# Optimization experiments

Measured on AMD Instinct MI355X. Metric: run time of the kernel, lower is better.

Reference implementation:

```python
import jax, jax.numpy as jnp
import numpy as np

B, C, H, W = 16, 512, 64, 64
K = 32


def setup_inputs() -> dict:
    key = jax.random.key(0)
    k1, k2, k3 = jax.random.split(key, 3)
    std = 1.0 / (64 * C) ** 0.5
    x = jax.random.normal(k1, (B, C, H, W), dtype=jnp.float32)
    codewords = jax.random.uniform(k2, (K, C), dtype=jnp.float32, minval=-std, maxval=std)
    scale = jax.random.uniform(k3, (K,), dtype=jnp.float32, minval=-1.0, maxval=0.0)
    return {"x": x, "codewords": codewords, "scale": scale}


def reference(x, codewords, scale):
    b, c, h, w = x.shape
    # (b, n, c) with n = h*w spatial positions
    xf = x.reshape(b, c, h * w).transpose(0, 2, 1)
    x2 = jnp.sum(xf * xf, axis=-1)                       # (b, n)
    c2 = jnp.sum(codewords * codewords, axis=-1)          # (k,)
    xc = jnp.einsum('bnc,kc->bnk', xf, codewords)         # (b, n, k)
    logits = scale[None, None, :] * (x2[:, :, None] - 2.0 * xc + c2[None, None, :])
    A = jax.nn.softmax(logits, axis=2)                    # (b, n, k)
    # sum_n A[b,n,k] * (x[b,n,c] - codewords[k,c])
    encoded = jnp.einsum('bnk,bnc->bkc', A, xf) - jnp.einsum('bnk,kc->bkc', A, codewords)
    return encoded
```

## Files before the change

kernel.cpp:

```cpp
#include <hip/hip_runtime.h>
#include <hip/hip_bf16.h>
#include <math.h>

#define BB 16
#define CC 512
#define NN 4096
#define KK 32

typedef __attribute__((ext_vector_type(8))) short short8;
typedef __attribute__((ext_vector_type(4))) float float4v;

static __device__ __forceinline__ unsigned short f2bf(float f) {
  unsigned u = __float_as_uint(f);
  u += 0x7FFF + ((u >> 16) & 1);
  return (unsigned short)(u >> 16);
}


__global__ __launch_bounds__(256) void prep_kernel(
    const float* __restrict__ cw, unsigned short* __restrict__ cwB,
    float* __restrict__ c2, float* __restrict__ asum, float* __restrict__ out) {
  int gid = blockIdx.x * 256 + threadIdx.x;
  float4v z = {0.f, 0.f, 0.f, 0.f};
  float4v* o4 = (float4v*)out;
#pragma unroll
  for (int j = 0; j < 4; ++j) o4[gid + j * 16384] = z;
  if (gid < BB * KK) asum[gid] = 0.f;
  cwB[gid] = f2bf(cw[gid]);
  __shared__ float c2p[KK][8];
  if (blockIdx.x == 0) {
    int k = threadIdx.x >> 3, j = threadIdx.x & 7;
    const float* row = cw + k * CC + j * 64;
    float s = 0.f;
    for (int i = 0; i < 64; ++i) s = fmaf(row[i], row[i], s);
    c2p[k][j] = s;
    __syncthreads();
    if (threadIdx.x < KK) {
      float t = 0.f;
      for (int j2 = 0; j2 < 8; ++j2) t += c2p[threadIdx.x][j2];
      c2[threadIdx.x] = t;
    }
  }
}

__global__ __launch_bounds__(256, 2) void logits_kernel(
    const float* __restrict__ x, const unsigned short* __restrict__ cwB,
    const float* __restrict__ c2g, const float* __restrict__ scale,
    unsigned short* __restrict__ A, float* __restrict__ asum) {
  const int b = blockIdx.x >> 6;
  const int n0 = (blockIdx.x & 63) << 6;
  const int t = threadIdx.x;

  __shared__ unsigned short Xl[512][68];
  __shared__ float Sx2p[16][68];
  __shared__ float Sx2[64];

  const float* xb = x + (size_t)b * CC * NN + n0;

  {
    const int f4 = t & 15;
    const int cr = t >> 4;
    float x2p0 = 0.f, x2p1 = 0.f, x2p2 = 0.f, x2p3 = 0.f;
    for (int cc = 0; cc < 512; cc += 64) {
      float4v v[4];
#pragma unroll
      for (int i = 0; i < 4; ++i)
        v[i] = *(const float4v*)(xb + (size_t)(cc + 16 * i + cr) * NN + 4 * f4);
#pragma unroll
      for (int i = 0; i < 4; ++i) {
        x2p0 = fmaf(v[i].x, v[i].x, x2p0);
        x2p1 = fmaf(v[i].y, v[i].y, x2p1);
        x2p2 = fmaf(v[i].z, v[i].z, x2p2);
        x2p3 = fmaf(v[i].w, v[i].w, x2p3);
        unsigned short h0 = f2bf(v[i].x), h1 = f2bf(v[i].y);
        unsigned short h2 = f2bf(v[i].z), h3 = f2bf(v[i].w);
        unsigned p0 = (unsigned)h0 | ((unsigned)h1 << 16);
        unsigned p1 = (unsigned)h2 | ((unsigned)h3 << 16);
        uint2 pk = make_uint2(p0, p1);
        *(uint2*)&Xl[cc + 16 * i + cr][4 * f4] = pk;
      }
    }
    Sx2p[cr][4 * f4 + 0] = x2p0;
    Sx2p[cr][4 * f4 + 1] = x2p1;
    Sx2p[cr][4 * f4 + 2] = x2p2;
    Sx2p[cr][4 * f4 + 3] = x2p3;
  }
  __syncthreads();
  if (t < 64) {
    float s = 0.f;
#pragma unroll
    for (int r = 0; r < 16; ++r) s += Sx2p[r][t];
    Sx2[t] = s;
  }
  __syncthreads();

  const int w = t >> 6;
  const int l = t & 63;
  const int l15 = l & 15;
  const int q = l >> 4;
  const int nrow = w * 16 + l15;

  float4v acc0 = {0.f, 0.f, 0.f, 0.f};
  float4v acc1 = {0.f, 0.f, 0.f, 0.f};

  for (int cs = 0; cs < 512; cs += 32) {
    const int cb = cs + q * 8;
    short8 af;
#pragma unroll
    for (int j = 0; j < 8; ++j) af[j] = (short)Xl[cb + j][nrow];
    short8 b0 = *(const short8*)(cwB + (size_t)l15 * CC + cb);
    short8 b1 = *(const short8*)(cwB + (size_t)(16 + l15) * CC + cb);
    acc0 = __builtin_amdgcn_mfma_f32_16x16x32_bf16(af, b0, acc0, 0, 0, 0);
    acc1 = __builtin_amdgcn_mfma_f32_16x16x32_bf16(af, b1, acc1, 0, 0, 0);
  }

  const float sc0 = scale[l15], sc1 = scale[16 + l15];
  const float cc0 = c2g[l15], cc1 = c2g[16 + l15];

  float a0[4], a1[4];
#pragma unroll
  for (int r = 0; r < 4; ++r) {
    const float xx = Sx2[w * 16 + 4 * q + r];
    float l0 = sc0 * (xx - 2.f * acc0[r] + cc0);
    float l1 = sc1 * (xx - 2.f * acc1[r] + cc1);
    float m = fmaxf(l0, l1);
    m = fmaxf(m, __shfl_xor(m, 1));
    m = fmaxf(m, __shfl_xor(m, 2));
    m = fmaxf(m, __shfl_xor(m, 4));
    m = fmaxf(m, __shfl_xor(m, 8));
    float e0 = __expf(l0 - m), e1 = __expf(l1 - m);
    float s = e0 + e1;
    s += __shfl_xor(s, 1);
    s += __shfl_xor(s, 2);
    s += __shfl_xor(s, 4);
    s += __shfl_xor(s, 8);
    float inv = 1.0f / s;
    a0[r] = e0 * inv;
    a1[r] = e1 * inv;
  }

  {
    unsigned p00 = (unsigned)f2bf(a0[0]) | ((unsigned)f2bf(a0[1]) << 16);
    unsigned p01 = (unsigned)f2bf(a0[2]) | ((unsigned)f2bf(a0[3]) << 16);
    unsigned p10 = (unsigned)f2bf(a1[0]) | ((unsigned)f2bf(a1[1]) << 16);
    unsigned p11 = (unsigned)f2bf(a1[2]) | ((unsigned)f2bf(a1[3]) << 16);
    unsigned short* A0 = A + ((size_t)(b * KK + l15)) * NN + n0 + w * 16 + 4 * q;
    unsigned short* A1 = A + ((size_t)(b * KK + 16 + l15)) * NN + n0 + w * 16 + 4 * q;
    *(uint2*)A0 = make_uint2(p00, p01);
    *(uint2*)A1 = make_uint2(p10, p11);
  }

  {
    float s0 = a0[0] + a0[1] + a0[2] + a0[3];
    float s1 = a1[0] + a1[1] + a1[2] + a1[3];
    s0 += __shfl_xor(s0, 16);
    s0 += __shfl_xor(s0, 32);
    s1 += __shfl_xor(s1, 16);
    s1 += __shfl_xor(s1, 32);
    if (q == 0) {
      atomicAdd(&asum[b * KK + l15], s0);
      atomicAdd(&asum[b * KK + 16 + l15], s1);
    }
  }
}

__global__ __launch_bounds__(256, 4) void agg_kernel(
    const float* __restrict__ x, const unsigned short* __restrict__ A,
    float* __restrict__ out) {
  const int b = blockIdx.x >> 6;
  const int cg = (blockIdx.x >> 4) & 3;
  const int n0 = (blockIdx.x & 15) << 8;
  const int t = threadIdx.x;
  const int w = t >> 6;
  const int l = t & 63;
  const int l15 = l & 15;
  const int q = l >> 4;
  const int cw0 = cg * 128 + 32 * w;

  float4v acc[2][2];
#pragma unroll
  for (int ct = 0; ct < 2; ++ct)
#pragma unroll
    for (int m = 0; m < 2; ++m) acc[ct][m] = (float4v){0.f, 0.f, 0.f, 0.f};

  const unsigned short* Ab = A + (size_t)b * KK * NN;
  const float* xb = x + (size_t)b * CC * NN;

  for (int s = 0; s < 8; ++s) {
    const int nb = n0 + s * 32 + q * 8;
    short8 a0 = *(const short8*)(Ab + (size_t)l15 * NN + nb);
    short8 a1 = *(const short8*)(Ab + (size_t)(16 + l15) * NN + nb);
#pragma unroll
    for (int ct = 0; ct < 2; ++ct) {
      const int c = cw0 + 16 * ct + l15;
      const float* xp = xb + (size_t)c * NN + nb;
      float4v x0 = *(const float4v*)xp;
      float4v x1 = *(const float4v*)(xp + 4);
      short8 bv;
      bv[0] = (short)f2bf(x0.x);
      bv[1] = (short)f2bf(x0.y);
      bv[2] = (short)f2bf(x0.z);
      bv[3] = (short)f2bf(x0.w);
      bv[4] = (short)f2bf(x1.x);
      bv[5] = (short)f2bf(x1.y);
      bv[6] = (short)f2bf(x1.z);
      bv[7] = (short)f2bf(x1.w);
      acc[ct][0] = __builtin_amdgcn_mfma_f32_16x16x32_bf16(a0, bv, acc[ct][0], 0, 0, 0);
      acc[ct][1] = __builtin_amdgcn_mfma_f32_16x16x32_bf16(a1, bv, acc[ct][1], 0, 0, 0);
    }
  }

#pragma unroll
  for (int ct = 0; ct < 2; ++ct) {
    const int c = cw0 + 16 * ct + l15;
#pragma unroll
    for (int m = 0; m < 2; ++m)
#pragma unroll
      for (int r = 0; r < 4; ++r) {
        int k = 16 * m + 4 * q + r;
        atomicAdd(&out[((size_t)(b * KK + k)) * CC + c], acc[ct][m][r]);
      }
  }
}

__global__ __launch_bounds__(256) void finalize_kernel(
    float* __restrict__ out, const float* __restrict__ asum,
    const float* __restrict__ cw) {
  int idx = blockIdx.x * 256 + threadIdx.x;
  int b = idx >> 12;
  int k = (idx >> 7) & 31;
  int c4 = idx & 127;
  float4v o = ((float4v*)out)[idx];
  float4v wv = ((const float4v*)cw)[k * 128 + c4];
  float a = asum[b * KK + k];
  o.x -= a * wv.x;
  o.y -= a * wv.y;
  o.z -= a * wv.z;
  o.w -= a * wv.w;
  ((float4v*)out)[idx] = o;
}

extern "C" void kernel_launch(void* const* d_in, const int* in_sizes, int n_in,
                              void* d_out, int out_size, void* d_ws, size_t ws_size,
                              hipStream_t stream) {
  const float* x = (const float*)d_in[0];
  const float* cw = (const float*)d_in[1];
  const float* scale = (const float*)d_in[2];
  float* out = (float*)d_out;
  char* ws = (char*)d_ws;

  float* c2 = (float*)ws;
  unsigned short* cwB = (unsigned short*)(ws + 128);
  float* asum = (float*)(ws + 32896);
  unsigned short* A = (unsigned short*)(ws + 34944);

  prep_kernel<<<64, 256, 0, stream>>>(cw, cwB, c2, asum, out);
  logits_kernel<<<1024, 256, 0, stream>>>(x, cwB, c2, scale, A, asum);
  agg_kernel<<<1024, 256, 0, stream>>>(x, A, out);
  finalize_kernel<<<256, 256, 0, stream>>>(out, asum, cw);
}
```

Before: 244.1 us.

## Fuse logits/softmax and aggregation into one kernel reusing bf16 x tile in LDS

Merges the logits/softmax kernel and the aggregation kernel into a single kernel. Each block processes 128 spatial positions in two sub-tiles of 64, keeps the bf16 x tile in shared memory and reuses it for both GEMMs, and stages the softmax weights in LDS. This removes the second full read of fp32 x and the global round trip of A. In exchange the grid is smaller (512 blocks), register pressure is higher from 16 accumulators per thread, the two phases are serialized by extra barriers, and there are more atomics per block on the output.

Result: faster. 233.0 us (-4.5%).

```diff
diff --git a/kernel.cpp b/kernel.cpp
--- a/kernel.cpp
+++ b/kernel.cpp
@@ -43,176 +43,136 @@
   }
 }
 
-__global__ __launch_bounds__(256, 2) void logits_kernel(
+#define XP 72
+__global__ __launch_bounds__(256, 2) void fused_kernel(
     const float* __restrict__ x, const unsigned short* __restrict__ cwB,
     const float* __restrict__ c2g, const float* __restrict__ scale,
-    unsigned short* __restrict__ A, float* __restrict__ asum) {
-  const int b = blockIdx.x >> 6;
-  const int n0 = (blockIdx.x & 63) << 6;
-  const int t = threadIdx.x;
-
-  __shared__ unsigned short Xl[512][68];
-  __shared__ float Sx2p[16][68];
-  __shared__ float Sx2[64];
-
-  const float* xb = x + (size_t)b * CC * NN + n0;
-
-  {
-    const int f4 = t & 15;
-    const int cr = t >> 4;
-    float x2p0 = 0.f, x2p1 = 0.f, x2p2 = 0.f, x2p3 = 0.f;
-    for (int cc = 0; cc < 512; cc += 64) {
-      float4v v[4];
-#pragma unroll
-      for (int i = 0; i < 4; ++i)
-        v[i] = *(const float4v*)(xb + (size_t)(cc + 16 * i + cr) * NN + 4 * f4);
-#pragma unroll
-      for (int i = 0; i < 4; ++i) {
-        x2p0 = fmaf(v[i].x, v[i].x, x2p0);
-        x2p1 = fmaf(v[i].y, v[i].y, x2p1);
-        x2p2 = fmaf(v[i].z, v[i].z, x2p2);
-        x2p3 = fmaf(v[i].w, v[i].w, x2p3);
-        unsigned short h0 = f2bf(v[i].x), h1 = f2bf(v[i].y);
-        unsigned short h2 = f2bf(v[i].z), h3 = f2bf(v[i].w);
-        unsigned p0 = (unsigned)h0 | ((unsigned)h1 << 16);
-        unsigned p1 = (unsigned)h2 | ((unsigned)h3 << 16);
-        uint2 pk = make_uint2(p0, p1);
-        *(uint2*)&Xl[cc + 16 * i + cr][4 * f4] = pk;
-      }
-    }
-    Sx2p[cr][4 * f4 + 0] = x2p0;
-    Sx2p[cr][4 * f4 + 1] = x2p1;
-    Sx2p[cr][4 * f4 + 2] = x2p2;
-    Sx2p[cr][4 * f4 + 3] = x2p3;
-  }
-  __syncthreads();
-  if (t < 64) {
-    float s = 0.f;
-#pragma unroll
-    for (int r = 0; r < 16; ++r) s += Sx2p[r][t];
-    Sx2[t] = s;
-  }
-  __syncthreads();
-
-  const int w = t >> 6;
-  const int l = t & 63;
-  const int l15 = l & 15;
-  const int q = l >> 4;
-  const int nrow = w * 16 + l15;
-
-  float4v acc0 = {0.f, 0.f, 0.f, 0.f};
-  float4v acc1 = {0.f, 0.f, 0.f, 0.f};
-
-  for (int cs = 0; cs < 512; cs += 32) {
-    const int cb = cs + q * 8;
-    short8 af;
-#pragma unroll
-    for (int j = 0; j < 8; ++j) af[j] = (short)Xl[cb + j][nrow];
-    short8 b0 = *(const short8*)(cwB + (size_t)l15 * CC + cb);
-    short8 b1 = *(const short8*)(cwB + (size_t)(16 + l15) * CC + cb);
-    acc0 = __builtin_amdgcn_mfma_f32_16x16x32_bf16(af, b0, acc0, 0, 0, 0);
-    acc1 = __builtin_amdgcn_mfma_f32_16x16x32_bf16(af, b1, acc1, 0, 0, 0);
-  }
-
-  const float sc0 = scale[l15], sc1 = scale[16 + l15];
-  const float cc0 = c2g[l15], cc1 = c2g[16 + l15];
-
-  float a0[4], a1[4];
-#pragma unroll
-  for (int r = 0; r < 4; ++r) {
-    const float xx = Sx2[w * 16 + 4 * q + r];
-    float l0 = sc0 * (xx - 2.f * acc0[r] + cc0);
-    float l1 = sc1 * (xx - 2.f * acc1[r] + cc1);
-    float m = fmaxf(l0, l1);
-    m = fmaxf(m, __shfl_xor(m, 1));
-    m = fmaxf(m, __shfl_xor(m, 2));
-    m = fmaxf(m, __shfl_xor(m, 4));
-    m = fmaxf(m, __shfl_xor(m, 8));
-    float e0 = __expf(l0 - m), e1 = __expf(l1 - m);
-    float s = e0 + e1;
-    s += __shfl_xor(s, 1);
-    s += __shfl_xor(s, 2);
-    s += __shfl_xor(s, 4);
-    s += __shfl_xor(s, 8);
-    float inv = 1.0f / s;
-    a0[r] = e0 * inv;
-    a1[r] = e1 * inv;
-  }
-
-  {
-    unsigned p00 = (unsigned)f2bf(a0[0]) | ((unsigned)f2bf(a0[1]) << 16);
-    unsigned p01 = (unsigned)f2bf(a0[2]) | ((unsigned)f2bf(a0[3]) << 16);
-    unsigned p10 = (unsigned)f2bf(a1[0]) | ((unsigned)f2bf(a1[1]) << 16);
-    unsigned p11 = (unsigned)f2bf(a1[2]) | ((unsigned)f2bf(a1[3]) << 16);
-    unsigned short* A0 = A + ((size_t)(b * KK + l15)) * NN + n0 + w * 16 + 4 * q;
-    unsigned short* A1 = A + ((size_t)(b * KK + 16 + l15)) * NN + n0 + w * 16 + 4 * q;
-    *(uint2*)A0 = make_uint2(p00, p01);
-    *(uint2*)A1 = make_uint2(p10, p11);
-  }
-
-  {
-    float s0 = a0[0] + a0[1] + a0[2] + a0[3];
-    float s1 = a1[0] + a1[1] + a1[2] + a1[3];
-    s0 += __shfl_xor(s0, 16);
-    s0 += __shfl_xor(s0, 32);
-    s1 += __shfl_xor(s1, 16);
-    s1 += __shfl_xor(s1, 32);
-    if (q == 0) {
-      atomicAdd(&asum[b * KK + l15], s0);
-      atomicAdd(&asum[b * KK + 16 + l15], s1);
-    }
-  }
-}
-
-__global__ __launch_bounds__(256, 4) void agg_kernel(
-    const float* __restrict__ x, const unsigned short* __restrict__ A,
-    float* __restrict__ out) {
-  const int b = blockIdx.x >> 6;
-  const int cg = (blockIdx.x >> 4) & 3;
-  const int n0 = (blockIdx.x & 15) << 8;
+    float* __restrict__ out, float* __restrict__ asum) {
+  const int b = blockIdx.x >> 5;
+  const int chunk = blockIdx.x & 31;
   const int t = threadIdx.x;
   const int w = t >> 6;
   const int l = t & 63;
   const int l15 = l & 15;
   const int q = l >> 4;
-  const int cw0 = cg * 128 + 32 * w;
-
-  float4v acc[2][2];
-#pragma unroll
-  for (int ct = 0; ct < 2; ++ct)
+
+  __shared__ char smem[512 * XP * 2 + 32 * XP * 2 + 256];
+  unsigned short* Xl = (unsigned short*)smem;
+  unsigned short* As = (unsigned short*)(smem + 512 * XP * 2);
+  float* Sx2p = (float*)(smem + 512 * XP * 2);
+  float* Sx2 = (float*)(smem + 512 * XP * 2 + 32 * XP * 2);
+
+  const float* xb0 = x + (size_t)b * CC * NN + chunk * 128;
+
+  const float sc0 = scale[l15], sc1 = scale[16 + l15];
+  const float cc0 = c2g[l15], cc1 = c2g[16 + l15];
+
+  float4v acc[8][2];
+#pragma unroll
+  for (int ct = 0; ct < 8; ++ct)
 #pragma unroll
     for (int m = 0; m < 2; ++m) acc[ct][m] = (float4v){0.f, 0.f, 0.f, 0.f};
-
-  const unsigned short* Ab = A + (size_t)b * KK * NN;
-  const float* xb = x + (size_t)b * CC * NN;
-
-  for (int s = 0; s < 8; ++s) {
-    const int nb = n0 + s * 32 + q * 8;
-    short8 a0 = *(const short8*)(Ab + (size_t)l15 * NN + nb);
-    short8 a1 = *(const short8*)(Ab + (size_t)(16 + l15) * NN + nb);
-#pragma unroll
-    for (int ct = 0; ct < 2; ++ct) {
-      const int c = cw0 + 16 * ct + l15;
-      const float* xp = xb + (size_t)c * NN + nb;
-      float4v x0 = *(const float4v*)xp;
-      float4v x1 = *(const float4v*)(xp + 4);
-      short8 bv;
-      bv[0] = (short)f2bf(x0.x);
-      bv[1] = (short)f2bf(x0.y);
-      bv[2] = (short)f2bf(x0.z);
-      bv[3] = (short)f2bf(x0.w);
-      bv[4] = (short)f2bf(x1.x);
-      bv[5] = (short)f2bf(x1.y);
-      bv[6] = (short)f2bf(x1.z);
-      bv[7] = (short)f2bf(x1.w);
-      acc[ct][0] = __builtin_amdgcn_mfma_f32_16x16x32_bf16(a0, bv, acc[ct][0], 0, 0, 0);
-      acc[ct][1] = __builtin_amdgcn_mfma_f32_16x16x32_bf16(a1, bv, acc[ct][1], 0, 0, 0);
-    }
-  }
-
-#pragma unroll
-  for (int ct = 0; ct < 2; ++ct) {
-    const int c = cw0 + 16 * ct + l15;
+  float s0acc = 0.f, s1acc = 0.f;
+
+  const int f4 = t & 15;
+  const int cr = t >> 4;
+
+  for (int sub = 0; sub < 2; ++sub) {
+    const float* xb = xb0 + sub * 64;
+
+    {
+      float4v x2p = {0.f, 0.f, 0.f, 0.f};
+#pragma unroll 8
+      for (int i = 0; i < 32; ++i) {
+        const int c = cr + 16 * i;
+        float4v v = *(const float4v*)(xb + (size_t)c * NN + 4 * f4);
+        x2p.x = fmaf(v.x, v.x, x2p.x);
+        x2p.y = fmaf(v.y, v.y, x2p.y);
+        x2p.z = fmaf(v.z, v.z, x2p.z);
+        x2p.w = fmaf(v.w, v.w, x2p.w);
+        unsigned p0 = (unsigned)f2bf(v.x) | ((unsigned)f2bf(v.y) << 16);
+        unsigned p1 = (unsigned)f2bf(v.z) | ((unsigned)f2bf(v.w) << 16);
+        *(uint2*)&Xl[c * XP + 4 * f4] = make_uint2(p0, p1);
+      }
+      *(float4v*)&Sx2p[cr * 68 + 4 * f4] = x2p;
+    }
+    __syncthreads();
+    if (t < 64) {
+      float s = 0.f;
+#pragma unroll
+      for (int r = 0; r < 16; ++r) s += Sx2p[r * 68 + t];
+      Sx2[t] = s;
+    }
+    __syncthreads();
+
+    float4v p0 = {0.f, 0.f, 0.f, 0.f};
+    float4v p1 = {0.f, 0.f, 0.f, 0.f};
+    const int nrow = w * 16 + l15;
+    for (int cs = 0; cs < 512; cs += 32) {
+      const int cb = cs + q * 8;
+      short8 af;
+#pragma unroll
+      for (int j = 0; j < 8; ++j) af[j] = (short)Xl[(cb + j) * XP + nrow];
+      short8 b0 = *(const short8*)(cwB + (size_t)l15 * CC + cb);
+      short8 b1 = *(const short8*)(cwB + (size_t)(16 + l15) * CC + cb);
+      p0 = __builtin_amdgcn_mfma_f32_16x16x32_bf16(af, b0, p0, 0, 0, 0);
+      p1 = __builtin_amdgcn_mfma_f32_16x16x32_bf16(af, b1, p1, 0, 0, 0);
+    }
+
+    float a0[4], a1[4];
+#pragma unroll
+    for (int r = 0; r < 4; ++r) {
+      const float xx = Sx2[w * 16 + 4 * q + r];
+      float l0 = sc0 * (xx - 2.f * p0[r] + cc0);
+      float l1 = sc1 * (xx - 2.f * p1[r] + cc1);
+      float m = fmaxf(l0, l1);
+      m = fmaxf(m, __shfl_xor(m, 1));
+      m = fmaxf(m, __shfl_xor(m, 2));
+      m = fmaxf(m, __shfl_xor(m, 4));
+      m = fmaxf(m, __shfl_xor(m, 8));
+      float e0 = __expf(l0 - m), e1 = __expf(l1 - m);
+      float s = e0 + e1;
+      s += __shfl_xor(s, 1);
+      s += __shfl_xor(s, 2);
+      s += __shfl_xor(s, 4);
+      s += __shfl_xor(s, 8);
+      float inv = 1.0f / s;
+      a0[r] = e0 * inv;
+      a1[r] = e1 * inv;
+    }
+    s0acc += a0[0] + a0[1] + a0[2] + a0[3];
+    s1acc += a1[0] + a1[1] + a1[2] + a1[3];
+
+    {
+      unsigned p00 = (unsigned)f2bf(a0[0]) | ((unsigned)f2bf(a0[1]) << 16);
+      unsigned p01 = (unsigned)f2bf(a0[2]) | ((unsigned)f2bf(a0[3]) << 16);
+      unsigned p10 = (unsigned)f2bf(a1[0]) | ((unsigned)f2bf(a1[1]) << 16);
+      unsigned p11 = (unsigned)f2bf(a1[2]) | ((unsigned)f2bf(a1[3]) << 16);
+      const int nc = w * 16 + 4 * q;
+      *(uint2*)&As[l15 * XP + nc] = make_uint2(p00, p01);
+      *(uint2*)&As[(16 + l15) * XP + nc] = make_uint2(p10, p11);
+    }
+    __syncthreads();
+
+#pragma unroll
+    for (int s = 0; s < 2; ++s) {
+      const int nb = s * 32 + q * 8;
+      short8 am0 = *(const short8*)&As[l15 * XP + nb];
+      short8 am1 = *(const short8*)&As[(16 + l15) * XP + nb];
+#pragma unroll
+      for (int ct = 0; ct < 8; ++ct) {
+        const int c = w * 128 + ct * 16 + l15;
+        short8 bx = *(const short8*)&Xl[c * XP + nb];
+        acc[ct][0] = __builtin_amdgcn_mfma_f32_16x16x32_bf16(am0, bx, acc[ct][0], 0, 0, 0);
+        acc[ct][1] = __builtin_amdgcn_mfma_f32_16x16x32_bf16(am1, bx, acc[ct][1], 0, 0, 0);
+      }
+    }
+    __syncthreads();
+  }
+
+#pragma unroll
+  for (int ct = 0; ct < 8; ++ct) {
+    const int c = w * 128 + ct * 16 + l15;
 #pragma unroll
     for (int m = 0; m < 2; ++m)
 #pragma unroll
@@ -220,6 +180,14 @@
         int k = 16 * m + 4 * q + r;
         atomicAdd(&out[((size_t)(b * KK + k)) * CC + c], acc[ct][m][r]);
       }
+  }
+  s0acc += __shfl_xor(s0acc, 16);
+  s0acc += __shfl_xor(s0acc, 32);
+  s1acc += __shfl_xor(s1acc, 16);
+  s1acc += __shfl_xor(s1acc, 32);
+  if (q == 0) {
+    atomicAdd(&asum[b * KK + l15], s0acc);
+    atomicAdd(&asum[b * KK + 16 + l15], s1acc);
   }
 }
 
@@ -252,10 +220,8 @@
   float* c2 = (float*)ws;
   unsigned short* cwB = (unsigned short*)(ws + 128);
   float* asum = (float*)(ws + 32896);
-  unsigned short* A = (unsigned short*)(ws + 34944);
 
   prep_kernel<<<64, 256, 0, stream>>>(cw, cwB, c2, asum, out);
-  logits_kernel<<<1024, 256, 0, stream>>>(x, cwB, c2, scale, A, asum);
-  agg_kernel<<<1024, 256, 0, stream>>>(x, A, out);
+  fused_kernel<<<512, 256, 0, stream>>>(x, cwB, c2, scale, out, asum);
   finalize_kernel<<<256, 256, 0, stream>>>(out, asum, cw);
 }
```
